# Kernel tuning notes

Hardware: AMD Instinct MI355X
Metric: run time of the kernel (lower is better)

The kernel has to match this reference:

```python
import jax, jax.numpy as jnp
import numpy as np

B, C, H, W, NH = 8, 512, 32, 32, 8
HD = C // NH
SCALE = HD ** -0.5


def reshape_for_attention(t, num_heads):
    # faithful to torch: view(B,nh,hd,HW) -> permute(0,3,1,2) -> view(B*nh, HW, hd)
    b, c, h, w = t.shape
    t = t.reshape(b, num_heads, c // num_heads, h * w)
    t = jnp.transpose(t, (0, 3, 1, 2))  # [B, HW, nh, hd]
    return t.reshape(b * num_heads, h * w, c // num_heads)


def reshape_from_attention(t, original_shape, num_heads):
    b, c, h, w = original_shape
    t = t.reshape(b, h * w, num_heads, c // num_heads)
    t = jnp.transpose(t, (0, 2, 3, 1))  # [B, nh, hd, HW]
    return t.reshape(b, c, h, w)


def setup_inputs() -> dict:
    key = jax.random.key(0)
    ks = jax.random.split(key, 6)
    s = (2.0 / C) ** 0.5  # kaiming-ish scale for 1x1 convs
    return {
        "x": jax.random.normal(ks[0], (B, C, H, W), dtype=jnp.float32),
        "wq": jax.random.normal(ks[1], (C, C), dtype=jnp.float32) * s,
        "wk": jax.random.normal(ks[2], (C, C), dtype=jnp.float32) * s,
        "wv": jax.random.normal(ks[3], (C, C), dtype=jnp.float32) * s,
        "wo": jax.random.normal(ks[4], (C, C), dtype=jnp.float32) * s,
        "ln_gamma": jnp.ones((C,), dtype=jnp.float32),
        "ln_beta": jnp.zeros((C,), dtype=jnp.float32),
        "gamma": jnp.zeros((1,), dtype=jnp.float32),
    }


def reference(x, wq, wk, wv, wo, ln_gamma, ln_beta, gamma):
    b, c, h, w = x.shape
    residual = x
    # 1x1 convs, no bias == channel GEMMs
    q = jnp.einsum('oc,bchw->bohw', wq, x)
    k = jnp.einsum('oc,bchw->bohw', wk, x)
    v = jnp.einsum('oc,bchw->bohw', wv, x)
    q = reshape_for_attention(q, NH)  # [B*nh, N, hd]
    k = reshape_for_attention(k, NH)
    v = reshape_for_attention(v, NH)
    attn = jnp.einsum('bnd,bmd->bnm', q, k) * SCALE  # [B*nh, N, N]
    attn = jax.nn.softmax(attn, axis=-1)
    attn_out = jnp.einsum('bnm,bmd->bnd', attn, v)
    attn_out = reshape_from_attention(attn_out, (b, c, h, w), NH)
    out = jnp.einsum('oc,bchw->bohw', wo, attn_out)
    # post-LN over channel dim
    out = jnp.transpose(out, (0, 2, 3, 1))  # [B,H,W,C]
    mu = jnp.mean(out, axis=-1, keepdims=True)
    var = jnp.var(out, axis=-1, keepdims=True)
    out = (out - mu) * jax.lax.rsqrt(var + 1e-5) * ln_gamma + ln_beta
    out = jnp.transpose(out, (0, 3, 1, 2))  # [B,C,H,W]
    return gamma * out + residual
```

## Files before the change

### kernel.cpp

```cpp
#include <hip/hip_runtime.h>
#include <hip/hip_bf16.h>


#define B_  8
#define C_  512
#define N_  1024
#define NH_ 8
#define HD_ 64

typedef __bf16 bf16x8 __attribute__((ext_vector_type(8)));
typedef __bf16 bf16x4 __attribute__((ext_vector_type(4)));
typedef float  f32x4  __attribute__((ext_vector_type(4)));

#define MFMA16(a, b, c) __builtin_amdgcn_mfma_f32_16x16x32_bf16((a), (b), (c), 0, 0, 0)

__device__ __forceinline__ void gload16(const void* g, void* l) {
    __builtin_amdgcn_global_load_lds(
        (const __attribute__((address_space(1))) unsigned int*)g,
        (__attribute__((address_space(3))) unsigned int*)l, 16, 0, 0);
}

__global__ __launch_bounds__(256) void k_prep(const float* __restrict__ x,
                                              const float* __restrict__ wq,
                                              const float* __restrict__ wk,
                                              const float* __restrict__ wv,
                                              const float* __restrict__ wo,
                                              __bf16* __restrict__ xt,
                                              __bf16* __restrict__ wcat) {
    __shared__ float tile[64][68];
    int blk = blockIdx.x;
    int tid = threadIdx.x;
    if (blk < 1024) {
        int b   = blk >> 7;
        int rem = blk & 127;
        int ct  = rem >> 4;
        int pt  = rem & 15;
        int c0 = ct * 64, p0 = pt * 64;
        for (int i = 0; i < 4; ++i) {
            int vi = i * 256 + tid;
            int c = vi >> 4, p4 = (vi & 15) * 4;
            f32x4 v = *(const f32x4*)(x + ((size_t)(b * C_ + c0 + c)) * N_ + p0 + p4);
            *(f32x4*)&tile[c][p4] = v;
        }
        __syncthreads();
        for (int i = 0; i < 4; ++i) {
            int vi = i * 256 + tid;
            int p = vi >> 4, c4 = (vi & 15) * 4;
            bf16x4 v;
            for (int j = 0; j < 4; ++j) v[j] = (__bf16)tile[c4 + j][p];
            *(bf16x4*)(xt + ((size_t)(b * N_ + p0 + p)) * C_ + c0 + c4) = v;
        }
    } else {
        int idx = (blk - 1024) * 256 + tid;
        int mat = idx >> 16;
        int off = (idx & 65535) * 4;
        const float* w = (mat == 0) ? wq : (mat == 1) ? wk : (mat == 2) ? wv : wo;
        f32x4 v = *(const f32x4*)(w + off);
        bf16x4 o;
        for (int j = 0; j < 4; ++j) o[j] = (__bf16)v[j];
        *(bf16x4*)(wcat + (size_t)mat * 262144 + off) = o;
    }
}

__global__ __launch_bounds__(256) void k_qkv(const __bf16* __restrict__ xt,
                                             const __bf16* __restrict__ wcat,
                                             __bf16* __restrict__ qa,
                                             __bf16* __restrict__ ka,
                                             __bf16* __restrict__ vt) {
    __shared__ __bf16 As[2][4096];
    __shared__ __bf16 Bs[2][4096];
    int blk  = blockIdx.x;
    int mat  = blk >> 8;
    int rem  = blk & 255;
    int b    = rem >> 5;
    int tile = rem & 31;
    int tid = threadIdx.x, lane = tid & 63, wid = tid >> 6;
    int quad = lane >> 4, l16 = lane & 15;

    const __bf16* w = wcat + (size_t)mat * 262144;
    const __bf16 *A, *Bm;
    int am0, bn0;
    if (mat < 2) {
        int mt = tile >> 2, nt = tile & 3;
        A   = xt + (size_t)b * N_ * C_;  am0 = mt * 128;
        Bm  = w;                         bn0 = nt * 128;
    } else {
        int mt = tile & 3, nt = tile >> 2;
        A   = w;                         am0 = mt * 128;
        Bm  = xt + (size_t)b * N_ * C_;  bn0 = nt * 128;
    }
    int wr = (wid >> 1) * 64, wc = (wid & 1) * 64;

    int lrow = wid * 16 + (lane >> 2);
    int scol = ((lane & 3) * 16) ^ ((lrow & 3) << 4);
    const char* aS0 = (const char*)A  + (size_t)(am0 + lrow) * 1024 + scol;
    const char* aS1 = aS0 + 65536;
    const char* bS0 = (const char*)Bm + (size_t)(bn0 + lrow) * 1024 + scol;
    const char* bS1 = bS0 + 65536;
    char* aD[2] = {(char*)&As[0][0] + wid * 1024, (char*)&As[1][0] + wid * 1024};
    char* bD[2] = {(char*)&Bs[0][0] + wid * 1024, (char*)&Bs[1][0] + wid * 1024};

    gload16(aS0, aD[0]);  gload16(aS1, aD[0] + 4096);
    gload16(bS0, bD[0]);  gload16(bS1, bD[0] + 4096);
    asm volatile("s_waitcnt vmcnt(0)" ::: "memory");
    __syncthreads();

    f32x4 acc[4][4] = {};
    const int fo = (quad * 16) ^ ((l16 & 3) << 4);
    int cur = 0;
    for (int t = 0; t < 16; ++t) {
        int kb = ((t + 1) & 15) * 64;
        gload16(aS0 + kb, aD[cur ^ 1]);  gload16(aS1 + kb, aD[cur ^ 1] + 4096);
        gload16(bS0 + kb, bD[cur ^ 1]);  gload16(bS1 + kb, bD[cur ^ 1] + 4096);

        const char* at = (const char*)&As[cur][0];
        const char* bt = (const char*)&Bs[cur][0];
        bf16x8 af[4], bfr[4];
        for (int i = 0; i < 4; ++i)
            af[i]  = *(const bf16x8*)(at + (wr + i * 16 + l16) * 64 + fo);
        for (int i = 0; i < 4; ++i)
            bfr[i] = *(const bf16x8*)(bt + (wc + i * 16 + l16) * 64 + fo);
        for (int mi = 0; mi < 4; ++mi)
            for (int ni = 0; ni < 4; ++ni)
                acc[mi][ni] = MFMA16(af[mi], bfr[ni], acc[mi][ni]);

        asm volatile("s_waitcnt vmcnt(0)" ::: "memory");
        __syncthreads();
        cur ^= 1;
    }

    if (mat < 2) {
        __bf16* dst = (mat == 0) ? qa : ka;
        for (int mi = 0; mi < 4; ++mi)
            for (int r = 0; r < 4; ++r) {
                int p = am0 + wr + mi * 16 + quad * 4 + r;
                int g = b * NH_ + (p >> 7);
                int nbase = (p & 127) * 8;
                for (int ni = 0; ni < 4; ++ni) {
                    int o = bn0 + wc + ni * 16 + l16;
                    dst[((size_t)g * N_ + nbase + (o >> 6)) * HD_ + (o & 63)] =
                        (__bf16)acc[mi][ni][r];
                }
            }
    } else {
        for (int mi = 0; mi < 4; ++mi)
            for (int r = 0; r < 4; ++r) {
                int o = am0 + wr + mi * 16 + quad * 4 + r;
                int m = o & 63, i = o >> 6;
                for (int ni = 0; ni < 4; ++ni) {
                    int p = bn0 + wc + ni * 16 + l16;
                    int g = b * NH_ + (p >> 7);
                    vt[((size_t)g * HD_ + m) * N_ + (p & 127) * 8 + i] =
                        (__bf16)acc[mi][ni][r];
                }
            }
    }
}

__global__ __launch_bounds__(256) void k_attn(const __bf16* __restrict__ qa,
                                              const __bf16* __restrict__ ka,
                                              const __bf16* __restrict__ vt,
                                              __bf16* __restrict__ ap) {
    __shared__ __bf16 Kb[2][4096];
    __shared__ __bf16 Vb[2][4096];
    __shared__ __bf16 plds[4][32][64];
    int blk = blockIdx.x;
    int g  = ((blk & 7) << 3) | ((blk >> 3) & 7);
    int qb = blk >> 6;
    int tid = threadIdx.x, lane = tid & 63, wid = tid >> 6;
    int quad = lane >> 4, l16 = lane & 15;
    int q0 = qb * 128 + wid * 32;

    const __bf16* qp = qa + (size_t)g * N_ * HD_;
    const char* kbb = (const char*)(ka + (size_t)g * N_ * HD_);
    const char* vbb = (const char*)(vt + (size_t)g * HD_ * N_);

    bf16x8 qA0 = *(const bf16x8*)(qp + (size_t)(q0 + l16) * HD_ + quad * 8);
    bf16x8 qA1 = *(const bf16x8*)(qp + (size_t)(q0 + l16) * HD_ + 32 + quad * 8);
    bf16x8 qB0 = *(const bf16x8*)(qp + (size_t)(q0 + 16 + l16) * HD_ + quad * 8);
    bf16x8 qB1 = *(const bf16x8*)(qp + (size_t)(q0 + 16 + l16) * HD_ + 32 + quad * 8);

    int lrow = lane >> 3;
    int scol = ((lane & 7) * 16) ^ (lrow << 4);
    const char* kSrc = kbb + (size_t)(wid * 16 + lrow) * 128  + scol;
    const char* vSrc = vbb + (size_t)(wid * 16 + lrow) * 2048 + scol;
    char* kds[2] = {(char*)&Kb[0][0] + wid * 2048, (char*)&Kb[1][0] + wid * 2048};
    char* vds[2] = {(char*)&Vb[0][0] + wid * 2048, (char*)&Vb[1][0] + wid * 2048};

    gload16(kSrc,          kds[0]);
    gload16(kSrc + 1024,   kds[0] + 1024);
    gload16(vSrc,          vds[0]);
    gload16(vSrc + 16384,  vds[0] + 1024);
    asm volatile("s_waitcnt vmcnt(0)" ::: "memory");
    __syncthreads();

    float liA = 0.f, liB = 0.f;
    f32x4 oA[4] = {}, oB[4] = {};
    const float sc = 0.125f * 1.44269504088896340736f;
    const int swzP = (l16 & 7) * 8;
    const int fsw  = (l16 & 7) << 4;

    int cur = 0;
    for (int t = 0; t < 16; ++t) {
        int jn = ((t + 1) & 15) * 64;
        gload16(kSrc + (size_t)jn * 128,          kds[cur ^ 1]);
        gload16(kSrc + (size_t)jn * 128 + 1024,   kds[cur ^ 1] + 1024);
        gload16(vSrc + jn * 2,                    vds[cur ^ 1]);
        gload16(vSrc + jn * 2 + 16384,            vds[cur ^ 1] + 1024);

        const char* kt = (const char*)&Kb[cur][0];
        bf16x8 kc0[4], kc1[4];
        for (int tt = 0; tt < 4; ++tt) {
            int rb = (tt * 16 + l16) * 128;
            kc0[tt] = *(const bf16x8*)(kt + rb + ((quad * 16) ^ fsw));
            kc1[tt] = *(const bf16x8*)(kt + rb + ((64 + quad * 16) ^ fsw));
        }
        f32x4 sA[4] = {}, sB[4] = {};
        for (int tt = 0; tt < 4; ++tt) {
            sA[tt] = MFMA16(kc0[tt], qA0, sA[tt]);
            sA[tt] = MFMA16(kc1[tt], qA1, sA[tt]);
            sB[tt] = MFMA16(kc0[tt], qB0, sB[tt]);
            sB[tt] = MFMA16(kc1[tt], qB1, sB[tt]);
        }

        for (int tt = 0; tt < 4; ++tt) {
            bf16x4 pkA, pkB;
            for (int r = 0; r < 4; ++r) {
                float pvA = exp2f(sA[tt][r] * sc);
                float pvB = exp2f(sB[tt][r] * sc);
                liA += pvA; liB += pvB;
                pkA[r] = (__bf16)pvA; pkB[r] = (__bf16)pvB;
            }
            int ks = (tt * 16 + quad * 4) ^ swzP;
            *(bf16x4*)&plds[wid][l16][ks]      = pkA;
            *(bf16x4*)&plds[wid][16 + l16][ks] = pkB;
        }

        asm volatile("" ::: "memory");
        const char* vtl = (const char*)&Vb[cur][0];
        for (int h = 0; h < 2; ++h) {
            int ks = (h * 32 + quad * 8) ^ swzP;
            bf16x8 pA = *(const bf16x8*)&plds[wid][l16][ks];
            bf16x8 pB = *(const bf16x8*)&plds[wid][16 + l16][ks];
            for (int dd = 0; dd < 4; ++dd) {
                bf16x8 av = *(const bf16x8*)(vtl + (dd * 16 + l16) * 128
                                             + ((h * 64 + quad * 16) ^ fsw));
                oA[dd] = MFMA16(av, pA, oA[dd]);
                oB[dd] = MFMA16(av, pB, oB[dd]);
            }
        }
        asm volatile("" ::: "memory");

        asm volatile("s_waitcnt vmcnt(0)" ::: "memory");
        __syncthreads();
        cur ^= 1;
    }

    liA += __shfl_xor(liA, 16, 64); liA += __shfl_xor(liA, 32, 64);
    liB += __shfl_xor(liB, 16, 64); liB += __shfl_xor(liB, 32, 64);

    int b = g >> 3, hi = g & 7;
    float invA = 1.0f / liA, invB = 1.0f / liB;
    int nA = q0 + l16, nB = q0 + 16 + l16;
    __bf16* dA = ap + ((size_t)(b * N_ + hi * 128 + (nA >> 3))) * C_ + (nA & 7) * 64;
    __bf16* dB = ap + ((size_t)(b * N_ + hi * 128 + (nB >> 3))) * C_ + (nB & 7) * 64;
    for (int dd = 0; dd < 4; ++dd) {
        bf16x4 oa, ob;
        for (int r = 0; r < 4; ++r) {
            oa[r] = (__bf16)(oA[dd][r] * invA);
            ob[r] = (__bf16)(oB[dd][r] * invB);
        }
        *(bf16x4*)(dA + dd * 16 + quad * 4) = oa;
        *(bf16x4*)(dB + dd * 16 + quad * 4) = ob;
    }
}

__global__ __launch_bounds__(256) void k_oproj(const __bf16* __restrict__ apm,
                                               const __bf16* __restrict__ wob,
                                               __bf16* __restrict__ o0) {
    __shared__ __bf16 As[2][4096];
    __shared__ __bf16 Bs[2][4096];
    int blk = blockIdx.x;
    int b = blk >> 5, tile = blk & 31;
    int mt = tile >> 2, nt = tile & 3;
    int tid = threadIdx.x, lane = tid & 63, wid = tid >> 6;
    int quad = lane >> 4, l16 = lane & 15;
    int am0 = mt * 128, bn0 = nt * 128;
    int wr = (wid >> 1) * 64, wc = (wid & 1) * 64;
    const __bf16* A = apm + (size_t)b * N_ * C_;

    int lrow = wid * 16 + (lane >> 2);
    int scol = ((lane & 3) * 16) ^ ((lrow & 3) << 4);
    const char* aS0 = (const char*)A   + (size_t)(am0 + lrow) * 1024 + scol;
    const char* aS1 = aS0 + 65536;
    const char* bS0 = (const char*)wob + (size_t)(bn0 + lrow) * 1024 + scol;
    const char* bS1 = bS0 + 65536;
    char* aD[2] = {(char*)&As[0][0] + wid * 1024, (char*)&As[1][0] + wid * 1024};
    char* bD[2] = {(char*)&Bs[0][0] + wid * 1024, (char*)&Bs[1][0] + wid * 1024};

    gload16(aS0, aD[0]);  gload16(aS1, aD[0] + 4096);
    gload16(bS0, bD[0]);  gload16(bS1, bD[0] + 4096);
    asm volatile("s_waitcnt vmcnt(0)" ::: "memory");
    __syncthreads();

    f32x4 acc[4][4] = {};
    const int fo = (quad * 16) ^ ((l16 & 3) << 4);
    int cur = 0;
    for (int t = 0; t < 16; ++t) {
        int kb = ((t + 1) & 15) * 64;
        gload16(aS0 + kb, aD[cur ^ 1]);  gload16(aS1 + kb, aD[cur ^ 1] + 4096);
        gload16(bS0 + kb, bD[cur ^ 1]);  gload16(bS1 + kb, bD[cur ^ 1] + 4096);

        const char* at = (const char*)&As[cur][0];
        const char* bt = (const char*)&Bs[cur][0];
        bf16x8 af[4], bfr[4];
        for (int i = 0; i < 4; ++i)
            af[i]  = *(const bf16x8*)(at + (wr + i * 16 + l16) * 64 + fo);
        for (int i = 0; i < 4; ++i)
            bfr[i] = *(const bf16x8*)(bt + (wc + i * 16 + l16) * 64 + fo);
        for (int mi = 0; mi < 4; ++mi)
            for (int ni = 0; ni < 4; ++ni)
                acc[mi][ni] = MFMA16(af[mi], bfr[ni], acc[mi][ni]);

        asm volatile("s_waitcnt vmcnt(0)" ::: "memory");
        __syncthreads();
        cur ^= 1;
    }
    for (int mi = 0; mi < 4; ++mi)
        for (int r = 0; r < 4; ++r) {
            int p = am0 + wr + mi * 16 + quad * 4 + r;
            __bf16* dst = o0 + ((size_t)(b * N_ + p)) * C_;
            for (int ni = 0; ni < 4; ++ni)
                dst[bn0 + wc + ni * 16 + l16] = (__bf16)acc[mi][ni][r];
        }
}

__global__ __launch_bounds__(256) void k_ln(const __bf16* __restrict__ o0,
                                            const float* __restrict__ x,
                                            const float* __restrict__ lng,
                                            const float* __restrict__ lnb,
                                            const float* __restrict__ gm,
                                            float* __restrict__ out) {
    __shared__ __bf16 tile[32][C_ + 4];
    int blk = blockIdx.x;
    int b = blk >> 5, pt = blk & 31;
    int p0 = pt * 32;
    int tid = threadIdx.x, lane = tid & 63, wid = tid >> 6;
    float g = gm[0];
    float lg[8], lb[8];
    *(f32x4*)&lg[0] = *(const f32x4*)(lng + lane * 8);
    *(f32x4*)&lg[4] = *(const f32x4*)(lng + lane * 8 + 4);
    *(f32x4*)&lb[0] = *(const f32x4*)(lnb + lane * 8);
    *(f32x4*)&lb[4] = *(const f32x4*)(lnb + lane * 8 + 4);

    for (int i = 0; i < 8; ++i) {
        int p = wid * 8 + i;
        bf16x8 v = *(const bf16x8*)(o0 + ((size_t)(b * N_ + p0 + p)) * C_ + lane * 8);
        float f[8], s = 0.f, ss = 0.f;
        for (int j = 0; j < 8; ++j) { f[j] = (float)v[j]; s += f[j]; ss += f[j] * f[j]; }
        for (int d = 1; d < 64; d <<= 1) { s += __shfl_xor(s, d, 64); ss += __shfl_xor(ss, d, 64); }
        float mean = s * (1.f / 512.f);
        float var  = ss * (1.f / 512.f) - mean * mean;
        float rstd = rsqrtf(fmaxf(var, 0.f) + 1e-5f);
        bf16x4 o1, o2;
        for (int j = 0; j < 4; ++j)
            o1[j] = (__bf16)(g * ((f[j] - mean) * rstd * lg[j] + lb[j]));
        for (int j = 0; j < 4; ++j)
            o2[j] = (__bf16)(g * ((f[j + 4] - mean) * rstd * lg[j + 4] + lb[j + 4]));
        __bf16* dst = &tile[p][lane * 8];
        *(bf16x4*)dst = o1;
        *(bf16x4*)(dst + 4) = o2;
    }
    __syncthreads();
    for (int it = 0; it < 16; ++it) {
        int task = it * 256 + tid;
        int c = task >> 3, p4 = (task & 7) * 4;
        f32x4 xr = *(const f32x4*)(x + ((size_t)(b * C_ + c)) * N_ + p0 + p4);
        f32x4 o;
        for (int j = 0; j < 4; ++j)
            o[j] = (float)tile[p4 + j][c] + xr[j];
        *(f32x4*)(out + ((size_t)(b * C_ + c)) * N_ + p0 + p4) = o;
    }
}

__global__ void k_qkv8f(const float* __restrict__ x, const float* __restrict__ wq,
                        const float* __restrict__ wk, const float* __restrict__ wv,
                        float* __restrict__ qa, float* __restrict__ ka,
                        float* __restrict__ va, int g0) {
    int idx = blockIdx.x * 256 + threadIdx.x;
    int m = idx & 63, n = (idx >> 6) & 1023, Gl = (idx >> 16) & 1, mat = idx >> 17;
    int G = g0 + Gl, b = G >> 3, hb = G & 7;
    int p = hb * 128 + (n >> 3), o = (n & 7) * 64 + m;
    const float* w = (mat == 0) ? wq : (mat == 1) ? wk : wv;
    float acc = 0.f;
    for (int c = 0; c < C_; ++c)
        acc += w[(size_t)o * C_ + c] * x[((size_t)b * C_ + c) * N_ + p];
    float* dst = (mat == 0) ? qa : (mat == 1) ? ka : va;
    dst[((size_t)Gl * N_ + n) * HD_ + m] = acc;
}
__global__ void k_attn8f(const float* __restrict__ qa, const float* __restrict__ ka,
                         const float* __restrict__ va, float* __restrict__ ac, int g0) {
    int idx = blockIdx.x * 256 + threadIdx.x;
    int i = idx & 1023, Gl = (idx >> 10) & 1, G = g0 + Gl;
    const float* qrow = qa + ((size_t)Gl * N_ + i) * HD_;
    float q[HD_];
    for (int m = 0; m < HD_; ++m) q[m] = qrow[m];
    const float* kb = ka + (size_t)Gl * N_ * HD_;
    const float* vb = va + (size_t)Gl * N_ * HD_;
    float mx = -1e30f;
    for (int j = 0; j < N_; ++j) {
        float s = 0.f;
        for (int m = 0; m < HD_; ++m) s += q[m] * kb[j * HD_ + m];
        mx = fmaxf(mx, s);
    }
    mx *= 0.125f;
    float l = 0.f, ov[HD_];
    for (int m = 0; m < HD_; ++m) ov[m] = 0.f;
    for (int j = 0; j < N_; ++j) {
        float s = 0.f;
        for (int m = 0; m < HD_; ++m) s += q[m] * kb[j * HD_ + m];
        float pj = __expf(s * 0.125f - mx);
        l += pj;
        for (int m = 0; m < HD_; ++m) ov[m] += pj * vb[j * HD_ + m];
    }
    float inv = 1.0f / l;
    int b = G >> 3, hb = G & 7;
    int p = hb * 128 + (i >> 3), cb = (i & 7) * 64;
    for (int m = 0; m < HD_; ++m)
        ac[((size_t)b * C_ + cb + m) * N_ + p] = ov[m] * inv;
}
__global__ void k_oln8f(float* __restrict__ ac, const float* __restrict__ wo,
                        const float* __restrict__ x, const float* __restrict__ lng,
                        const float* __restrict__ lnb, const float* __restrict__ gm) {
    int tid = threadIdx.x, lane = tid & 63, wid = tid >> 6;
    int bp = blockIdx.x * 4 + wid;
    int b = bp >> 10, p = bp & 1023;
    float oc[8];
    for (int h = 0; h < 8; ++h) oc[h] = 0.f;
    for (int c = 0; c < C_; ++c) {
        float cv = ac[((size_t)b * C_ + c) * N_ + p];
        for (int h = 0; h < 8; ++h)
            oc[h] += wo[(size_t)(h * 64 + lane) * C_ + c] * cv;
    }
    float s = 0.f, ss = 0.f;
    for (int h = 0; h < 8; ++h) { s += oc[h]; ss += oc[h] * oc[h]; }
    for (int d = 1; d < 64; d <<= 1) { s += __shfl_xor(s, d, 64); ss += __shfl_xor(ss, d, 64); }
    float mean = s * (1.f / 512.f);
    float var  = ss * (1.f / 512.f) - mean * mean;
    float rstd = rsqrtf(fmaxf(var, 0.f) + 1e-5f);
    float g = gm[0];
    for (int h = 0; h < 8; ++h) {
        int o = h * 64 + lane;
        float xv = x[((size_t)b * C_ + o) * N_ + p];
        ac[((size_t)b * C_ + o) * N_ + p] =
            g * ((oc[h] - mean) * rstd * lng[o] + lnb[o]) + xv;
    }
}

extern "C" void kernel_launch(void* const* d_in, const int* in_sizes, int n_in,
                              void* d_out, int out_size, void* d_ws, size_t ws_size,
                              hipStream_t stream) {
    const float* x   = (const float*)d_in[0];
    const float* wq  = (const float*)d_in[1];
    const float* wk  = (const float*)d_in[2];
    const float* wv  = (const float*)d_in[3];
    const float* wo  = (const float*)d_in[4];
    const float* lng = (const float*)d_in[5];
    const float* lnb = (const float*)d_in[6];
    const float* gm  = (const float*)d_in[7];
    float* out = (float*)d_out;
    char* wsb = (char*)d_ws;

    if (ws_size >= ((size_t)18 << 20)) {
        __bf16* xt   = (__bf16*)wsb;
        __bf16* wcat = (__bf16*)(wsb + ((size_t)8 << 20));
        __bf16* Qa   = (__bf16*)(wsb + ((size_t)10 << 20));
        __bf16* Ka   = (__bf16*)d_out;
        __bf16* VaT  = (__bf16*)((char*)d_out + ((size_t)8 << 20));
        __bf16* ap   = xt;
        __bf16* o0   = Qa;
        __bf16* wob  = wcat + 3 * 262144;

        k_prep  <<<2048, 256, 0, stream>>>(x, wq, wk, wv, wo, xt, wcat);
        k_qkv   <<<768,  256, 0, stream>>>(xt, wcat, Qa, Ka, VaT);
        k_attn  <<<512,  256, 0, stream>>>(Qa, Ka, VaT, ap);
        k_oproj <<<256,  256, 0, stream>>>(ap, wob, o0);
        k_ln    <<<256,  256, 0, stream>>>(o0, x, lng, lnb, gm, out);
    } else {
        float* qa = (float*)(wsb + 256);
        float* ka = qa + 2 * N_ * HD_;
        float* va = ka + 2 * N_ * HD_;
        for (int g0 = 0; g0 < 64; g0 += 2) {
            k_qkv8f <<<1536, 256, 0, stream>>>(x, wq, wk, wv, qa, ka, va, g0);
            k_attn8f<<<8,    256, 0, stream>>>(qa, ka, va, out, g0);
        }
        k_oln8f<<<2048, 256, 0, stream>>>(out, wo, x, lng, lnb, gm);
    }
}
```

Before: 166.4 us.

## Triple-buffer LDS tiles with prefetch distance two in GEMM and attention kernels

Switches the QKV GEMM, attention and output-projection kernels from double to triple LDS buffering. Loads are issued two tiles ahead, and the wait uses vmcnt(4) instead of vmcnt(0), so one tile's global-to-LDS loads can stay in flight across the barrier. This aims to hide more global latency behind MFMA work. The cost is 50% more LDS per block for the staging buffers, which may reduce occupancy, and it relies on the compiler emitting no extra vector memory operations between the waits.

```diff
diff --git a/kernel.cpp b/kernel.cpp
--- a/kernel.cpp
+++ b/kernel.cpp
@@ -67,8 +67,8 @@
                                              __bf16* __restrict__ qa,
                                              __bf16* __restrict__ ka,
                                              __bf16* __restrict__ vt) {
-    __shared__ __bf16 As[2][4096];
-    __shared__ __bf16 Bs[2][4096];
+    __shared__ __bf16 As[3][4096];
+    __shared__ __bf16 Bs[3][4096];
     int blk  = blockIdx.x;
     int mat  = blk >> 8;
     int rem  = blk & 255;
@@ -97,36 +97,38 @@
     const char* aS1 = aS0 + 65536;
     const char* bS0 = (const char*)Bm + (size_t)(bn0 + lrow) * 1024 + scol;
     const char* bS1 = bS0 + 65536;
-    char* aD[2] = {(char*)&As[0][0] + wid * 1024, (char*)&As[1][0] + wid * 1024};
-    char* bD[2] = {(char*)&Bs[0][0] + wid * 1024, (char*)&Bs[1][0] + wid * 1024};
-
-    gload16(aS0, aD[0]);  gload16(aS1, aD[0] + 4096);
-    gload16(bS0, bD[0]);  gload16(bS1, bD[0] + 4096);
-    asm volatile("s_waitcnt vmcnt(0)" ::: "memory");
-    __syncthreads();
+    int wb = wid * 1024;
+
+    char *aR = (char*)&As[0][0], *aN = (char*)&As[1][0], *aP = (char*)&As[2][0];
+    char *bR = (char*)&Bs[0][0], *bN = (char*)&Bs[1][0], *bP = (char*)&Bs[2][0];
+
+    gload16(aS0,      aR + wb);  gload16(aS1,      aR + wb + 4096);
+    gload16(bS0,      bR + wb);  gload16(bS1,      bR + wb + 4096);
+    gload16(aS0 + 64, aN + wb);  gload16(aS1 + 64, aN + wb + 4096);
+    gload16(bS0 + 64, bN + wb);  gload16(bS1 + 64, bN + wb + 4096);
+    asm volatile("s_waitcnt vmcnt(4)" ::: "memory");
+    __builtin_amdgcn_s_barrier();
 
     f32x4 acc[4][4] = {};
     const int fo = (quad * 16) ^ ((l16 & 3) << 4);
-    int cur = 0;
     for (int t = 0; t < 16; ++t) {
-        int kb = ((t + 1) & 15) * 64;
-        gload16(aS0 + kb, aD[cur ^ 1]);  gload16(aS1 + kb, aD[cur ^ 1] + 4096);
-        gload16(bS0 + kb, bD[cur ^ 1]);  gload16(bS1 + kb, bD[cur ^ 1] + 4096);
-
-        const char* at = (const char*)&As[cur][0];
-        const char* bt = (const char*)&Bs[cur][0];
+        int kb = ((t + 2) & 15) * 64;
+        gload16(aS0 + kb, aP + wb);  gload16(aS1 + kb, aP + wb + 4096);
+        gload16(bS0 + kb, bP + wb);  gload16(bS1 + kb, bP + wb + 4096);
+
         bf16x8 af[4], bfr[4];
         for (int i = 0; i < 4; ++i)
-            af[i]  = *(const bf16x8*)(at + (wr + i * 16 + l16) * 64 + fo);
+            af[i]  = *(const bf16x8*)(aR + (wr + i * 16 + l16) * 64 + fo);
         for (int i = 0; i < 4; ++i)
-            bfr[i] = *(const bf16x8*)(bt + (wc + i * 16 + l16) * 64 + fo);
+            bfr[i] = *(const bf16x8*)(bR + (wc + i * 16 + l16) * 64 + fo);
         for (int mi = 0; mi < 4; ++mi)
             for (int ni = 0; ni < 4; ++ni)
                 acc[mi][ni] = MFMA16(af[mi], bfr[ni], acc[mi][ni]);
 
-        asm volatile("s_waitcnt vmcnt(0)" ::: "memory");
-        __syncthreads();
-        cur ^= 1;
+        asm volatile("s_waitcnt vmcnt(4)" ::: "memory");
+        __builtin_amdgcn_s_barrier();
+        char* ta = aR; aR = aN; aN = aP; aP = ta;
+        char* tb = bR; bR = bN; bN = bP; bP = tb;
     }
 
     if (mat < 2) {
@@ -161,8 +163,8 @@
                                               const __bf16* __restrict__ ka,
                                               const __bf16* __restrict__ vt,
                                               __bf16* __restrict__ ap) {
-    __shared__ __bf16 Kb[2][4096];
-    __shared__ __bf16 Vb[2][4096];
+    __shared__ __bf16 Kb[3][4096];
+    __shared__ __bf16 Vb[3][4096];
     __shared__ __bf16 plds[4][32][64];
     int blk = blockIdx.x;
     int g  = ((blk & 7) << 3) | ((blk >> 3) & 7);
@@ -184,15 +186,21 @@
     int scol = ((lane & 7) * 16) ^ (lrow << 4);
     const char* kSrc = kbb + (size_t)(wid * 16 + lrow) * 128  + scol;
     const char* vSrc = vbb + (size_t)(wid * 16 + lrow) * 2048 + scol;
-    char* kds[2] = {(char*)&Kb[0][0] + wid * 2048, (char*)&Kb[1][0] + wid * 2048};
-    char* vds[2] = {(char*)&Vb[0][0] + wid * 2048, (char*)&Vb[1][0] + wid * 2048};
-
-    gload16(kSrc,          kds[0]);
-    gload16(kSrc + 1024,   kds[0] + 1024);
-    gload16(vSrc,          vds[0]);
-    gload16(vSrc + 16384,  vds[0] + 1024);
-    asm volatile("s_waitcnt vmcnt(0)" ::: "memory");
-    __syncthreads();
+    int wb = wid * 2048;
+
+    char *kR = (char*)&Kb[0][0], *kN = (char*)&Kb[1][0], *kP = (char*)&Kb[2][0];
+    char *vR = (char*)&Vb[0][0], *vN = (char*)&Vb[1][0], *vP = (char*)&Vb[2][0];
+
+    gload16(kSrc,                 kR + wb);
+    gload16(kSrc + 1024,          kR + wb + 1024);
+    gload16(vSrc,                 vR + wb);
+    gload16(vSrc + 16384,         vR + wb + 1024);
+    gload16(kSrc + 8192,          kN + wb);
+    gload16(kSrc + 8192 + 1024,   kN + wb + 1024);
+    gload16(vSrc + 128,           vN + wb);
+    gload16(vSrc + 128 + 16384,   vN + wb + 1024);
+    asm volatile("s_waitcnt vmcnt(4)" ::: "memory");
+    __builtin_amdgcn_s_barrier();
 
     float liA = 0.f, liB = 0.f;
     f32x4 oA[4] = {}, oB[4] = {};
@@ -200,20 +208,18 @@
     const int swzP = (l16 & 7) * 8;
     const int fsw  = (l16 & 7) << 4;
 
-    int cur = 0;
     for (int t = 0; t < 16; ++t) {
-        int jn = ((t + 1) & 15) * 64;
-        gload16(kSrc + (size_t)jn * 128,          kds[cur ^ 1]);
-        gload16(kSrc + (size_t)jn * 128 + 1024,   kds[cur ^ 1] + 1024);
-        gload16(vSrc + jn * 2,                    vds[cur ^ 1]);
-        gload16(vSrc + jn * 2 + 16384,            vds[cur ^ 1] + 1024);
-
-        const char* kt = (const char*)&Kb[cur][0];
+        int jn = ((t + 2) & 15) * 64;
+        gload16(kSrc + (size_t)jn * 128,          kP + wb);
+        gload16(kSrc + (size_t)jn * 128 + 1024,   kP + wb + 1024);
+        gload16(vSrc + jn * 2,                    vP + wb);
+        gload16(vSrc + jn * 2 + 16384,            vP + wb + 1024);
+
         bf16x8 kc0[4], kc1[4];
         for (int tt = 0; tt < 4; ++tt) {
             int rb = (tt * 16 + l16) * 128;
-            kc0[tt] = *(const bf16x8*)(kt + rb + ((quad * 16) ^ fsw));
-            kc1[tt] = *(const bf16x8*)(kt + rb + ((64 + quad * 16) ^ fsw));
+            kc0[tt] = *(const bf16x8*)(kR + rb + ((quad * 16) ^ fsw));
+            kc1[tt] = *(const bf16x8*)(kR + rb + ((64 + quad * 16) ^ fsw));
         }
         f32x4 sA[4] = {}, sB[4] = {};
         for (int tt = 0; tt < 4; ++tt) {
@@ -237,13 +243,12 @@
         }
 
         asm volatile("" ::: "memory");
-        const char* vtl = (const char*)&Vb[cur][0];
         for (int h = 0; h < 2; ++h) {
             int ks = (h * 32 + quad * 8) ^ swzP;
             bf16x8 pA = *(const bf16x8*)&plds[wid][l16][ks];
             bf16x8 pB = *(const bf16x8*)&plds[wid][16 + l16][ks];
             for (int dd = 0; dd < 4; ++dd) {
-                bf16x8 av = *(const bf16x8*)(vtl + (dd * 16 + l16) * 128
+                bf16x8 av = *(const bf16x8*)(vR + (dd * 16 + l16) * 128
                                              + ((h * 64 + quad * 16) ^ fsw));
                 oA[dd] = MFMA16(av, pA, oA[dd]);
                 oB[dd] = MFMA16(av, pB, oB[dd]);
@@ -251,9 +256,10 @@
         }
         asm volatile("" ::: "memory");
 
-        asm volatile("s_waitcnt vmcnt(0)" ::: "memory");
-        __syncthreads();
-        cur ^= 1;
+        asm volatile("s_waitcnt vmcnt(4)" ::: "memory");
+        __builtin_amdgcn_s_barrier();
+        char* tk = kR; kR = kN; kN = kP; kP = tk;
+        char* tv = vR; vR = vN; vN = vP; vP = tv;
     }
 
     liA += __shfl_xor(liA, 16, 64); liA += __shfl_xor(liA, 32, 64);
@@ -278,8 +284,8 @@
 __global__ __launch_bounds__(256) void k_oproj(const __bf16* __restrict__ apm,
                                                const __bf16* __restrict__ wob,
                                                __bf16* __restrict__ o0) {
-    __shared__ __bf16 As[2][4096];
-    __shared__ __bf16 Bs[2][4096];
+    __shared__ __bf16 As[3][4096];
+    __shared__ __bf16 Bs[3][4096];
     int blk = blockIdx.x;
     int b = blk >> 5, tile = blk & 31;
     int mt = tile >> 2, nt = tile & 3;
@@ -295,36 +301,38 @@
     const char* aS1 = aS0 + 65536;
     const char* bS0 = (const char*)wob + (size_t)(bn0 + lrow) * 1024 + scol;
     const char* bS1 = bS0 + 65536;
-    char* aD[2] = {(char*)&As[0][0] + wid * 1024, (char*)&As[1][0] + wid * 1024};
-    char* bD[2] = {(char*)&Bs[0][0] + wid * 1024, (char*)&Bs[1][0] + wid * 1024};
-
-    gload16(aS0, aD[0]);  gload16(aS1, aD[0] + 4096);
-    gload16(bS0, bD[0]);  gload16(bS1, bD[0] + 4096);
-    asm volatile("s_waitcnt vmcnt(0)" ::: "memory");
-    __syncthreads();
+    int wb = wid * 1024;
+
+    char *aR = (char*)&As[0][0], *aN = (char*)&As[1][0], *aP = (char*)&As[2][0];
+    char *bR = (char*)&Bs[0][0], *bN = (char*)&Bs[1][0], *bP = (char*)&Bs[2][0];
+
+    gload16(aS0,      aR + wb);  gload16(aS1,      aR + wb + 4096);
+    gload16(bS0,      bR + wb);  gload16(bS1,      bR + wb + 4096);
+    gload16(aS0 + 64, aN + wb);  gload16(aS1 + 64, aN + wb + 4096);
+    gload16(bS0 + 64, bN + wb);  gload16(bS1 + 64, bN + wb + 4096);
+    asm volatile("s_waitcnt vmcnt(4)" ::: "memory");
+    __builtin_amdgcn_s_barrier();
 
     f32x4 acc[4][4] = {};
     const int fo = (quad * 16) ^ ((l16 & 3) << 4);
-    int cur = 0;
     for (int t = 0; t < 16; ++t) {
-        int kb = ((t + 1) & 15) * 64;
-        gload16(aS0 + kb, aD[cur ^ 1]);  gload16(aS1 + kb, aD[cur ^ 1] + 4096);
-        gload16(bS0 + kb, bD[cur ^ 1]);  gload16(bS1 + kb, bD[cur ^ 1] + 4096);
-
-        const char* at = (const char*)&As[cur][0];
-        const char* bt = (const char*)&Bs[cur][0];
+        int kb = ((t + 2) & 15) * 64;
+        gload16(aS0 + kb, aP + wb);  gload16(aS1 + kb, aP + wb + 4096);
+        gload16(bS0 + kb, bP + wb);  gload16(bS1 + kb, bP + wb + 4096);
+
         bf16x8 af[4], bfr[4];
         for (int i = 0; i < 4; ++i)
-            af[i]  = *(const bf16x8*)(at + (wr + i * 16 + l16) * 64 + fo);
+            af[i]  = *(const bf16x8*)(aR + (wr + i * 16 + l16) * 64 + fo);
         for (int i = 0; i < 4; ++i)
-            bfr[i] = *(const bf16x8*)(bt + (wc + i * 16 + l16) * 64 + fo);
+            bfr[i] = *(const bf16x8*)(bR + (wc + i * 16 + l16) * 64 + fo);
         for (int mi = 0; mi < 4; ++mi)
             for (int ni = 0; ni < 4; ++ni)
                 acc[mi][ni] = MFMA16(af[mi], bfr[ni], acc[mi][ni]);
 
-        asm volatile("s_waitcnt vmcnt(0)" ::: "memory");
-        __syncthreads();
-        cur ^= 1;
+        asm volatile("s_waitcnt vmcnt(4)" ::: "memory");
+        __builtin_amdgcn_s_barrier();
+        char* ta = aR; aR = aN; aN = aP; aP = ta;
+        char* tb = bR; bR = bN; bN = bP; bP = tb;
     }
     for (int mi = 0; mi < 4; ++mi)
         for (int r = 0; r < 4; ++r) {
```

Measured after the change: 168.1 us. About the same (+1.0%).
